# Kernel optimization log

Hardware: AMD Instinct MI355X
Metric: run time of the kernel (lower is better)

Reference implementation:

```python
import math
import jax, jax.numpy as jnp
import numpy as np

GRID_SIZE = 17
GRID_RANGE = 2.5
WIDTHS = [128, 256, 128]
LN_EPS = 1e-5

GRID = jnp.linspace(-GRID_RANGE, GRID_RANGE, GRID_SIZE, dtype=jnp.float32)
SPACING = jnp.float32(2.0 * GRID_RANGE / (GRID_SIZE - 1))


def _kan_layer(x, base_scale, spline_w, bias):
    # x: (B, I); base_scale: (I, O); spline_w: (I, O, G); bias: (O,)
    I = x.shape[-1]
    # degree-1 (hat) spline basis: (B, I, G)
    basis = jnp.clip(1.0 - jnp.abs(x[..., None] - GRID) / SPACING, 0.0, None)
    spline = jnp.einsum('big,iog->bio', basis, spline_w)          # (B, I, O)
    base = jax.nn.silu(x)[..., None] * base_scale[None]            # (B, I, O)
    edge = base + spline                                           # (B, I, O)
    out = edge.sum(axis=1) / math.sqrt(float(I)) + bias            # (B, O)
    return out, edge, basis


def _layer_norm(x, gamma, beta):
    mu = x.mean(axis=-1, keepdims=True)
    var = ((x - mu) ** 2).mean(axis=-1, keepdims=True)
    return (x - mu) * jax.lax.rsqrt(var + LN_EPS) * gamma + beta


def setup_inputs() -> dict:
    key = jax.random.key(0)
    ks = jax.random.split(key, 8)
    B = 4096
    I0, H, O = WIDTHS
    fan0 = 1.0 / math.sqrt(float(I0))
    fan1 = 1.0 / math.sqrt(float(H))
    return {
        'x': jax.random.normal(ks[0], (B, I0), dtype=jnp.float32),
        'base_scale0': fan0 * jax.random.normal(ks[1], (I0, H), dtype=jnp.float32),
        'spline_w0': 0.1 * fan0 * jax.random.normal(ks[2], (I0, H, GRID_SIZE), dtype=jnp.float32),
        'bias0': jnp.zeros((H,), dtype=jnp.float32),
        'base_scale1': fan1 * jax.random.normal(ks[3], (H, O), dtype=jnp.float32),
        'spline_w1': 0.1 * fan1 * jax.random.normal(ks[4], (H, O, GRID_SIZE), dtype=jnp.float32),
        'bias1': jnp.zeros((O,), dtype=jnp.float32),
        'ln_gamma': jnp.ones((H,), dtype=jnp.float32),
        'ln_beta': jnp.zeros((H,), dtype=jnp.float32),
    }


def reference(x, base_scale0, spline_w0, bias0, base_scale1, spline_w1, bias1, ln_gamma, ln_beta):
    h, _, _ = _kan_layer(x, base_scale0, spline_w0, bias0)
    h = _layer_norm(h, ln_gamma, ln_beta)
    out, edge1, basis1 = _kan_layer(h, base_scale1, spline_w1, bias1)
    # diagnostics on the last layer (mean/std, std unbiased=False)
    se_mean = edge1.mean()
    se_std = edge1.std()
    sb_mean = basis1.mean()
    sb_std = basis1.std()
    return out, edge1, basis1, se_mean, se_std, sb_mean, sb_std
```

## Files before the change

kernel.cpp:

```cpp
#include <hip/hip_runtime.h>

#define BATCH 4096
#define NI 128
#define NH 256
#define NO 128
#define NG 17

static constexpr size_t EDGE_OFF  = (size_t)BATCH * NO;
static constexpr size_t BASIS_OFF = EDGE_OFF + (size_t)BATCH * NH * NO;
static constexpr size_t SCAL_OFF  = BASIS_OFF + (size_t)BATCH * NH * NG;

typedef float  vf2 __attribute__((ext_vector_type(2)));
typedef float  vf4 __attribute__((ext_vector_type(4)));

__device__ __forceinline__ unsigned short f2bf(float v) {
    unsigned int b = __float_as_uint(v);
    b += 0x7FFFu + ((b >> 16) & 1u);
    return (unsigned short)(b >> 16);
}
__device__ __forceinline__ float bf2f(unsigned short u) {
    return __uint_as_float((unsigned int)u << 16);
}
__device__ __forceinline__ float2 bf2_to_f2(unsigned int v) {
    float2 r;
    r.x = __uint_as_float(v << 16);
    r.y = __uint_as_float(v & 0xFFFF0000u);
    return r;
}
__device__ __forceinline__ float4 bf4_to_f4(uint2 v) {
    float4 r;
    r.x = __uint_as_float(v.x << 16);
    r.y = __uint_as_float(v.x & 0xFFFF0000u);
    r.z = __uint_as_float(v.y << 16);
    r.w = __uint_as_float(v.y & 0xFFFF0000u);
    return r;
}

__device__ __forceinline__ void taps(float v, float& sil, float& wlo, float& whi,
                                     int& glo, int& ghi, float& u) {
    sil = v / (1.0f + __expf(-v));
    u   = (v + 2.5f) * 3.2f;
    float kf = floorf(u);
    int   k  = (int)kf;
    float f  = u - kf;
    wlo = 1.0f - f;  whi = f;
    glo = k;         ghi = k + 1;
    if (glo < 0 || glo > 16) { glo = 0; wlo = 0.0f; }
    if (ghi < 0 || ghi > 16) { ghi = 0; whi = 0.0f; }
}

__global__ __launch_bounds__(256) void transpose_convert(
    const float* __restrict__ w0, const float* __restrict__ w1,
    const float* __restrict__ bs1,
    unsigned short* __restrict__ w0t, unsigned short* __restrict__ w1t,
    unsigned short* __restrict__ bs1b) {
    int j = blockIdx.x * 256 + threadIdx.x;
    const int total0 = NI * NG * NH;
    const int total1 = NH * NG * NO;
    if (j < total0) {
        int i = j / (NG * NH);
        int r = j - i * (NG * NH);
        int g = r / NH;
        int o = r - g * NH;
        w0t[j] = f2bf(w0[((size_t)i * NH + o) * NG + g]);
    } else if (j < total0 + total1) {
        int jj = j - total0;
        int i = jj / (NG * NO);
        int r = jj - i * (NG * NO);
        int g = r / NO;
        int o = r - g * NO;
        w1t[jj] = f2bf(w1[((size_t)i * NO + o) * NG + g]);
    } else {
        int jj = j - total0 - total1;
        bs1b[jj] = f2bf(bs1[jj]);
    }
}

__global__ __launch_bounds__(128) void kan_fused(
    const float* __restrict__ x,
    const float* __restrict__ bs0,
    const float* __restrict__ bias0,
    const unsigned short* __restrict__ bs1,
    const float* __restrict__ bias1,
    const float* __restrict__ gamma,
    const float* __restrict__ beta,
    const unsigned short* __restrict__ w0t,
    const unsigned short* __restrict__ w1t,
    float* __restrict__ out,
    float4* __restrict__ partials)
{
    __shared__ float s_sil0[NI], s_wlo0[NI], s_whi0[NI];
    __shared__ int   s_gp0[NI];
    __shared__ float s_sil1[NH], s_wlo1[NH], s_whi1[NH], s_u1[NH];
    __shared__ int   s_glo1[NH], s_ghi1[NH];
    __shared__ float s_red[128];
    __shared__ float4 s_out4[128];
    __shared__ float4 s_red4[128];

    const int tid = threadIdx.x;
    const int b   = blockIdx.x;

    {
        float xv = x[(size_t)b * NI + tid];
        float sil, wlo, whi, u; int glo, ghi;
        taps(xv, sil, wlo, whi, glo, ghi, u);
        s_sil0[tid] = sil; s_wlo0[tid] = wlo; s_whi0[tid] = whi;
        s_gp0[tid] = glo | (ghi << 8);
    }
    __syncthreads();

    const int op = tid * 2;
    float h0 = 0.0f, h1 = 0.0f;
    for (int i = 0; i < NI; ++i) {
        const float sil = s_sil0[i], wlo = s_wlo0[i], whi = s_whi0[i];
        const unsigned int gp = (unsigned int)s_gp0[i];
        const float2 bsv = *reinterpret_cast<const float2*>(bs0 + (size_t)i * NH + op);
        const float2 wl  = bf2_to_f2(*reinterpret_cast<const unsigned int*>(w0t + ((size_t)i * NG + (gp & 0xffu)) * NH + op));
        const float2 wh  = bf2_to_f2(*reinterpret_cast<const unsigned int*>(w0t + ((size_t)i * NG + (gp >> 8)) * NH + op));
        h0 += sil * bsv.x + wlo * wl.x + whi * wh.x;
        h1 += sil * bsv.y + wlo * wl.y + whi * wh.y;
    }
    {
        const float2 b0 = *reinterpret_cast<const float2*>(bias0 + op);
        h0 = h0 * 0.08838834764831844f + b0.x;
        h1 = h1 * 0.08838834764831844f + b0.y;
    }

    s_red[tid] = h0 + h1;
    __syncthreads();
    for (int s = 64; s > 0; s >>= 1) {
        if (tid < s) s_red[tid] += s_red[tid + s];
        __syncthreads();
    }
    const float mu = s_red[0] * (1.0f / NH);
    __syncthreads();
    const float d0 = h0 - mu, d1 = h1 - mu;
    s_red[tid] = d0 * d0 + d1 * d1;
    __syncthreads();
    for (int s = 64; s > 0; s >>= 1) {
        if (tid < s) s_red[tid] += s_red[tid + s];
        __syncthreads();
    }
    const float rs = rsqrtf(s_red[0] * (1.0f / NH) + 1e-5f);
    __syncthreads();
    float hn0, hn1;
    {
        const float2 gm = *reinterpret_cast<const float2*>(gamma + op);
        const float2 bt = *reinterpret_cast<const float2*>(beta + op);
        hn0 = d0 * rs * gm.x + bt.x;
        hn1 = d1 * rs * gm.y + bt.y;
    }

    float bsum, bsq;
    {
        float sil, wlo, whi, u; int glo, ghi;
        taps(hn0, sil, wlo, whi, glo, ghi, u);
        s_sil1[op] = sil; s_wlo1[op] = wlo; s_whi1[op] = whi;
        s_glo1[op] = glo; s_ghi1[op] = ghi; s_u1[op] = u;
        bsum = wlo + whi;  bsq = wlo * wlo + whi * whi;
        taps(hn1, sil, wlo, whi, glo, ghi, u);
        s_sil1[op + 1] = sil; s_wlo1[op + 1] = wlo; s_whi1[op + 1] = whi;
        s_glo1[op + 1] = glo; s_ghi1[op + 1] = ghi; s_u1[op + 1] = u;
        bsum += wlo + whi; bsq += wlo * wlo + whi * whi;
    }
    __syncthreads();

    {
        float* bo = out + BASIS_OFF + (size_t)b * (NH * NG);
        #pragma unroll
        for (int it = 0; it < 17; ++it) {
            int f0 = (it * 128 + tid) * 2;
            int i0 = f0 / NG,       g0 = f0 - i0 * NG;
            int i1 = (f0 + 1) / NG, g1 = (f0 + 1) - i1 * NG;
            vf2 v;
            v.x = fmaxf(0.0f, 1.0f - fabsf(s_u1[i0] - (float)g0));
            v.y = fmaxf(0.0f, 1.0f - fabsf(s_u1[i1] - (float)g1));
            __builtin_nontemporal_store(v, reinterpret_cast<vf2*>(bo + f0));
        }
    }

    const int po = (tid & 31) * 4;
    const int q  = tid >> 5;
    float4 osum = make_float4(0.f, 0.f, 0.f, 0.f);
    float esq = 0.0f;
    float* eo = out + EDGE_OFF + (size_t)b * (NH * NO);
    #pragma unroll 2
    for (int it = 0; it < 64; ++it) {
        const int i = q * 64 + it;
        const float sil = s_sil1[i], wlo = s_wlo1[i], whi = s_whi1[i];
        const float4 bsv = bf4_to_f4(*reinterpret_cast<const uint2*>(bs1 + (size_t)i * NO + po));
        const float4 wl  = bf4_to_f4(*reinterpret_cast<const uint2*>(w1t + (size_t)(i * NG + s_glo1[i]) * NO + po));
        const float4 wh  = bf4_to_f4(*reinterpret_cast<const uint2*>(w1t + (size_t)(i * NG + s_ghi1[i]) * NO + po));
        vf4 e;
        e.x = sil * bsv.x + wlo * wl.x + whi * wh.x;
        e.y = sil * bsv.y + wlo * wl.y + whi * wh.y;
        e.z = sil * bsv.z + wlo * wl.z + whi * wh.z;
        e.w = sil * bsv.w + wlo * wl.w + whi * wh.w;
        __builtin_nontemporal_store(e, reinterpret_cast<vf4*>(eo + (size_t)i * NO + po));
        osum.x += e.x; osum.y += e.y; osum.z += e.z; osum.w += e.w;
        esq += e.x * e.x + e.y * e.y + e.z * e.z + e.w * e.w;
    }

    s_out4[tid] = osum;
    __syncthreads();
    if (tid < 32) {
        float4 a = s_out4[tid], b2 = s_out4[tid + 32], c = s_out4[tid + 64], d2 = s_out4[tid + 96];
        const float4 bi = *reinterpret_cast<const float4*>(bias1 + tid * 4);
        float4 o4;
        o4.x = (a.x + b2.x + c.x + d2.x) * 0.0625f + bi.x;
        o4.y = (a.y + b2.y + c.y + d2.y) * 0.0625f + bi.y;
        o4.z = (a.z + b2.z + c.z + d2.z) * 0.0625f + bi.z;
        o4.w = (a.w + b2.w + c.w + d2.w) * 0.0625f + bi.w;
        *reinterpret_cast<float4*>(out + (size_t)b * NO + tid * 4) = o4;
    }

    s_red4[tid] = make_float4(osum.x + osum.y + osum.z + osum.w, esq, bsum, bsq);
    __syncthreads();
    for (int s = 64; s > 0; s >>= 1) {
        if (tid < s) {
            float4 a = s_red4[tid], c = s_red4[tid + s];
            s_red4[tid] = make_float4(a.x + c.x, a.y + c.y, a.z + c.z, a.w + c.w);
        }
        __syncthreads();
    }
    if (tid == 0) partials[b] = s_red4[0];
}

__global__ __launch_bounds__(256) void finalize(const float4* __restrict__ partials,
                                                float* __restrict__ out) {
    __shared__ double red[256];
    const int tid = threadIdx.x;
    double a0 = 0, a1 = 0, a2 = 0, a3 = 0;
    for (int j = tid; j < BATCH; j += 256) {
        float4 p = partials[j];
        a0 += (double)p.x; a1 += (double)p.y; a2 += (double)p.z; a3 += (double)p.w;
    }
    double tot[4];
    double v[4] = {a0, a1, a2, a3};
    for (int c = 0; c < 4; ++c) {
        red[tid] = v[c];
        __syncthreads();
        for (int s = 128; s > 0; s >>= 1) {
            if (tid < s) red[tid] += red[tid + s];
            __syncthreads();
        }
        tot[c] = red[0];
        __syncthreads();
    }
    if (tid == 0) {
        const double Ne = (double)BATCH * NH * NO;
        const double Nb = (double)BATCH * NH * NG;
        double me = tot[0] / Ne;
        double ve = tot[1] / Ne - me * me;
        double mb = tot[2] / Nb;
        double vb = tot[3] / Nb - mb * mb;
        out[SCAL_OFF + 0] = (float)me;
        out[SCAL_OFF + 1] = (float)sqrt(ve > 0.0 ? ve : 0.0);
        out[SCAL_OFF + 2] = (float)mb;
        out[SCAL_OFF + 3] = (float)sqrt(vb > 0.0 ? vb : 0.0);
    }
}

extern "C" void kernel_launch(void* const* d_in, const int* in_sizes, int n_in,
                              void* d_out, int out_size, void* d_ws, size_t ws_size,
                              hipStream_t stream) {
    const float* x     = (const float*)d_in[0];
    const float* bs0   = (const float*)d_in[1];
    const float* w0    = (const float*)d_in[2];
    const float* bias0 = (const float*)d_in[3];
    const float* bs1   = (const float*)d_in[4];
    const float* w1    = (const float*)d_in[5];
    const float* bias1 = (const float*)d_in[6];
    const float* gamma = (const float*)d_in[7];
    const float* beta  = (const float*)d_in[8];
    float* out = (float*)d_out;

    unsigned short* w0t  = (unsigned short*)d_ws;
    unsigned short* w1t  = w0t + (size_t)NI * NG * NH;
    unsigned short* bs1b = w1t + (size_t)NH * NG * NO;
    size_t ofs = ((size_t)(NI * NG * NH) + (size_t)(NH * NG * NO) + NH * NO) * sizeof(unsigned short);
    ofs = (ofs + 15) & ~(size_t)15;
    float4* partials = (float4*)((char*)d_ws + ofs);

    hipLaunchKernelGGL(transpose_convert, dim3(4480), dim3(256), 0, stream,
                       w0, w1, bs1, w0t, w1t, bs1b);
    hipLaunchKernelGGL(kan_fused, dim3(BATCH), dim3(128), 0, stream,
                       x, bs0, bias0, bs1b, bias1, gamma, beta, w0t, w1t, out, partials);
    hipLaunchKernelGGL(finalize, dim3(1), dim3(256), 0, stream, partials, out);
}
```

Measured before the change: 166.0 us.

## Split fused KAN kernel into layer-0 and edge kernels via workspace buffer

Splits the single fused kernel into two launches. The first computes layer 0 plus LayerNorm and writes the normalized hidden vector to a workspace buffer. The second reads it back and computes the layer-1 edges, basis and partials. The aim is to lower per-kernel register and shared-memory pressure so each kernel can reach higher occupancy. The cost is an extra launch and a small global round trip for the hidden activations. The hidden-index mapping is also changed from interleaved pairs to tid and tid+128.

Result: slower. 173.7 us (+4.6%).

```diff
diff --git a/kernel.cpp b/kernel.cpp
--- a/kernel.cpp
+++ b/kernel.cpp
@@ -17,9 +17,6 @@
     unsigned int b = __float_as_uint(v);
     b += 0x7FFFu + ((b >> 16) & 1u);
     return (unsigned short)(b >> 16);
-}
-__device__ __forceinline__ float bf2f(unsigned short u) {
-    return __uint_as_float((unsigned int)u << 16);
 }
 __device__ __forceinline__ float2 bf2_to_f2(unsigned int v) {
     float2 r;
@@ -76,26 +73,18 @@
     }
 }
 
-__global__ __launch_bounds__(128) void kan_fused(
+__global__ __launch_bounds__(128) void kan_l0(
     const float* __restrict__ x,
     const float* __restrict__ bs0,
     const float* __restrict__ bias0,
-    const unsigned short* __restrict__ bs1,
-    const float* __restrict__ bias1,
     const float* __restrict__ gamma,
     const float* __restrict__ beta,
     const unsigned short* __restrict__ w0t,
-    const unsigned short* __restrict__ w1t,
-    float* __restrict__ out,
-    float4* __restrict__ partials)
+    float* __restrict__ hn)
 {
     __shared__ float s_sil0[NI], s_wlo0[NI], s_whi0[NI];
     __shared__ int   s_gp0[NI];
-    __shared__ float s_sil1[NH], s_wlo1[NH], s_whi1[NH], s_u1[NH];
-    __shared__ int   s_glo1[NH], s_ghi1[NH];
     __shared__ float s_red[128];
-    __shared__ float4 s_out4[128];
-    __shared__ float4 s_red4[128];
 
     const int tid = threadIdx.x;
     const int b   = blockIdx.x;
@@ -143,24 +132,44 @@
     }
     const float rs = rsqrtf(s_red[0] * (1.0f / NH) + 1e-5f);
     __syncthreads();
-    float hn0, hn1;
     {
         const float2 gm = *reinterpret_cast<const float2*>(gamma + op);
         const float2 bt = *reinterpret_cast<const float2*>(beta + op);
-        hn0 = d0 * rs * gm.x + bt.x;
-        hn1 = d1 * rs * gm.y + bt.y;
-    }
-
+        vf2 o;
+        o.x = d0 * rs * gm.x + bt.x;
+        o.y = d1 * rs * gm.y + bt.y;
+        *reinterpret_cast<vf2*>(hn + (size_t)b * NH + op) = o;
+    }
+}
+
+__global__ __launch_bounds__(128) void kan_edge(
+    const float* __restrict__ hn,
+    const unsigned short* __restrict__ bs1,
+    const float* __restrict__ bias1,
+    const unsigned short* __restrict__ w1t,
+    float* __restrict__ out,
+    float4* __restrict__ partials)
+{
+    __shared__ float s_sil1[NH], s_wlo1[NH], s_whi1[NH], s_u1[NH];
+    __shared__ int   s_glo1[NH], s_ghi1[NH];
+    __shared__ float4 s_out4[128];
+    __shared__ float4 s_red4[128];
+
+    const int tid = threadIdx.x;
+    const int b   = blockIdx.x;
+
+    const float hn0 = hn[(size_t)b * NH + tid];
+    const float hn1 = hn[(size_t)b * NH + tid + 128];
     float bsum, bsq;
     {
         float sil, wlo, whi, u; int glo, ghi;
         taps(hn0, sil, wlo, whi, glo, ghi, u);
-        s_sil1[op] = sil; s_wlo1[op] = wlo; s_whi1[op] = whi;
-        s_glo1[op] = glo; s_ghi1[op] = ghi; s_u1[op] = u;
+        s_sil1[tid] = sil; s_wlo1[tid] = wlo; s_whi1[tid] = whi;
+        s_glo1[tid] = glo; s_ghi1[tid] = ghi; s_u1[tid] = u;
         bsum = wlo + whi;  bsq = wlo * wlo + whi * whi;
         taps(hn1, sil, wlo, whi, glo, ghi, u);
-        s_sil1[op + 1] = sil; s_wlo1[op + 1] = wlo; s_whi1[op + 1] = whi;
-        s_glo1[op + 1] = glo; s_ghi1[op + 1] = ghi; s_u1[op + 1] = u;
+        s_sil1[tid + 128] = sil; s_wlo1[tid + 128] = wlo; s_whi1[tid + 128] = whi;
+        s_glo1[tid + 128] = glo; s_ghi1[tid + 128] = ghi; s_u1[tid + 128] = u;
         bsum += wlo + whi; bsq += wlo * wlo + whi * whi;
     }
     __syncthreads();
@@ -281,10 +290,13 @@
     size_t ofs = ((size_t)(NI * NG * NH) + (size_t)(NH * NG * NO) + NH * NO) * sizeof(unsigned short);
     ofs = (ofs + 15) & ~(size_t)15;
     float4* partials = (float4*)((char*)d_ws + ofs);
+    float*  hnbuf    = (float*)((char*)d_ws + ofs + BATCH * sizeof(float4));
 
     hipLaunchKernelGGL(transpose_convert, dim3(4480), dim3(256), 0, stream,
                        w0, w1, bs1, w0t, w1t, bs1b);
-    hipLaunchKernelGGL(kan_fused, dim3(BATCH), dim3(128), 0, stream,
-                       x, bs0, bias0, bs1b, bias1, gamma, beta, w0t, w1t, out, partials);
+    hipLaunchKernelGGL(kan_l0, dim3(BATCH), dim3(128), 0, stream,
+                       x, bs0, bias0, gamma, beta, w0t, hnbuf);
+    hipLaunchKernelGGL(kan_edge, dim3(BATCH), dim3(128), 0, stream,
+                       hnbuf, bs1b, bias1, w1t, out, partials);
     hipLaunchKernelGGL(finalize, dim3(1), dim3(256), 0, stream, partials, out);
 }
```

## Split layer 0 into a dense MFMA GEMM over the full hat-basis expansion

Applied to the files above, without the earlier changes.

Layer 0 is moved out of the per-row fused kernel into a new kernel. It handles 16 batch rows per block, builds the dense 128x17 hat-basis matrix on the fly in bf16 and multiplies it against pre-tiled bf16 spline weights using MFMA 16x16x32 instructions. The SiLU base term is computed with fp32 FMAs, and the result is written to a workspace buffer that the fused kernel reads back. This swaps sparse two-tap gathers, which reload the weights for every row, for dense matrix-core work with reuse across 16 rows. The cost is one extra launch, a global round trip for the hidden activations, bf16 rounding of the basis values, and many MFMAs on zero basis entries.

After: 179.7 us. 1.08x slower.

```diff
diff --git a/kernel.cpp b/kernel.cpp
--- a/kernel.cpp
+++ b/kernel.cpp
@@ -5,6 +5,7 @@
 #define NH 256
 #define NO 128
 #define NG 17
+#define K0 2176
 
 static constexpr size_t EDGE_OFF  = (size_t)BATCH * NO;
 static constexpr size_t BASIS_OFF = EDGE_OFF + (size_t)BATCH * NH * NO;
@@ -12,20 +13,13 @@
 
 typedef float  vf2 __attribute__((ext_vector_type(2)));
 typedef float  vf4 __attribute__((ext_vector_type(4)));
+typedef short  bf16x8 __attribute__((ext_vector_type(8)));
+typedef float  f32x4 __attribute__((ext_vector_type(4)));
 
 __device__ __forceinline__ unsigned short f2bf(float v) {
     unsigned int b = __float_as_uint(v);
     b += 0x7FFFu + ((b >> 16) & 1u);
     return (unsigned short)(b >> 16);
-}
-__device__ __forceinline__ float bf2f(unsigned short u) {
-    return __uint_as_float((unsigned int)u << 16);
-}
-__device__ __forceinline__ float2 bf2_to_f2(unsigned int v) {
-    float2 r;
-    r.x = __uint_as_float(v << 16);
-    r.y = __uint_as_float(v & 0xFFFF0000u);
-    return r;
 }
 __device__ __forceinline__ float4 bf4_to_f4(uint2 v) {
     float4 r;
@@ -52,45 +46,112 @@
 __global__ __launch_bounds__(256) void transpose_convert(
     const float* __restrict__ w0, const float* __restrict__ w1,
     const float* __restrict__ bs1,
-    unsigned short* __restrict__ w0t, unsigned short* __restrict__ w1t,
+    unsigned short* __restrict__ w0B, unsigned short* __restrict__ w1t,
     unsigned short* __restrict__ bs1b) {
     int j = blockIdx.x * 256 + threadIdx.x;
-    const int total0 = NI * NG * NH;
+    const int n0 = K0 / 32 * NH;
     const int total1 = NH * NG * NO;
-    if (j < total0) {
-        int i = j / (NG * NH);
-        int r = j - i * (NG * NH);
-        int g = r / NH;
-        int o = r - g * NH;
-        w0t[j] = f2bf(w0[((size_t)i * NH + o) * NG + g]);
-    } else if (j < total0 + total1) {
-        int jj = j - total0;
+    if (j < n0) {
+        const int kt = j >> 8;
+        const int o  = j & 255;
+        unsigned short* dst = w0B + (size_t)kt * 8192 + o * 32;
+        #pragma unroll
+        for (int kl = 0; kl < 32; ++kl) {
+            unsigned int k = kt * 32 + kl;
+            unsigned int i = (k * 3856u) >> 16;
+            unsigned int g = k - 17u * i;
+            dst[kl] = f2bf(w0[((size_t)i * NH + o) * NG + g]);
+        }
+    } else if (j < n0 + total1) {
+        int jj = j - n0;
         int i = jj / (NG * NO);
         int r = jj - i * (NG * NO);
         int g = r / NO;
         int o = r - g * NO;
         w1t[jj] = f2bf(w1[((size_t)i * NO + o) * NG + g]);
-    } else {
-        int jj = j - total0 - total1;
+    } else if (j < n0 + total1 + NH * NO) {
+        int jj = j - n0 - total1;
         bs1b[jj] = f2bf(bs1[jj]);
     }
 }
 
-__global__ __launch_bounds__(128) void kan_fused(
+__global__ __launch_bounds__(512) void layer0_gemm(
     const float* __restrict__ x,
     const float* __restrict__ bs0,
+    const unsigned short* __restrict__ w0B,
+    float* __restrict__ hsum)
+{
+    __shared__ float s_u[16 * 129];
+    __shared__ float s_sil[16 * NI];
+    __shared__ float s_hb[16 * NH];
+    const int tid = threadIdx.x;
+    const int rb  = blockIdx.x * 16;
+
+    for (int j = tid; j < 16 * NI; j += 512) {
+        const int r = j >> 7, c = j & 127;
+        float xv = x[(size_t)rb * NI + j];
+        s_sil[j] = xv / (1.0f + __expf(-xv));
+        s_u[r * 129 + c] = (xv + 2.5f) * 3.2f;
+    }
+    __syncthreads();
+
+    {
+        const int o  = tid & 255;
+        const int r0 = (tid >> 8) * 8;
+        float acc[8] = {};
+        #pragma unroll 4
+        for (int k = 0; k < NI; ++k) {
+            float bv = bs0[(size_t)k * NH + o];
+            #pragma unroll
+            for (int r = 0; r < 8; ++r) acc[r] += s_sil[(r0 + r) * NI + k] * bv;
+        }
+        #pragma unroll
+        for (int r = 0; r < 8; ++r) s_hb[(r0 + r) * NH + o] = acc[r];
+    }
+    __syncthreads();
+
+    const int lane = tid & 63;
+    const int wave = tid >> 6;
+    const int r    = lane & 15;
+    const int kg   = lane >> 4;
+    const int o0   = (wave * 2 + 0) * 16 + (lane & 15);
+    const int o1   = (wave * 2 + 1) * 16 + (lane & 15);
+    f32x4 acc0 = {0.f, 0.f, 0.f, 0.f}, acc1 = {0.f, 0.f, 0.f, 0.f};
+    for (int kt = 0; kt < K0 / 32; ++kt) {
+        const int k0 = kt * 32 + kg * 8;
+        bf16x8 av;
+        #pragma unroll
+        for (int j = 0; j < 8; ++j) {
+            unsigned int k = k0 + j;
+            unsigned int i = (k * 3856u) >> 16;
+            float g = (float)(k - 17u * i);
+            float v = fmaxf(0.0f, 1.0f - fabsf(s_u[r * 129 + i] - g));
+            av[j] = (short)f2bf(v);
+        }
+        const bf16x8 bv0 = *reinterpret_cast<const bf16x8*>(w0B + (size_t)kt * 8192 + o0 * 32 + kg * 8);
+        const bf16x8 bv1 = *reinterpret_cast<const bf16x8*>(w0B + (size_t)kt * 8192 + o1 * 32 + kg * 8);
+        acc0 = __builtin_amdgcn_mfma_f32_16x16x32_bf16(av, bv0, acc0, 0, 0, 0);
+        acc1 = __builtin_amdgcn_mfma_f32_16x16x32_bf16(av, bv1, acc1, 0, 0, 0);
+    }
+    #pragma unroll
+    for (int reg = 0; reg < 4; ++reg) {
+        const int row = kg * 4 + reg;
+        hsum[(size_t)(rb + row) * NH + o0] = acc0[reg] + s_hb[row * NH + o0];
+        hsum[(size_t)(rb + row) * NH + o1] = acc1[reg] + s_hb[row * NH + o1];
+    }
+}
+
+__global__ __launch_bounds__(128) void kan_fused(
+    const float* __restrict__ hsum,
     const float* __restrict__ bias0,
     const unsigned short* __restrict__ bs1,
     const float* __restrict__ bias1,
     const float* __restrict__ gamma,
     const float* __restrict__ beta,
-    const unsigned short* __restrict__ w0t,
     const unsigned short* __restrict__ w1t,
     float* __restrict__ out,
     float4* __restrict__ partials)
 {
-    __shared__ float s_sil0[NI], s_wlo0[NI], s_whi0[NI];
-    __shared__ int   s_gp0[NI];
     __shared__ float s_sil1[NH], s_wlo1[NH], s_whi1[NH], s_u1[NH];
     __shared__ int   s_glo1[NH], s_ghi1[NH];
     __shared__ float s_red[128];
@@ -100,30 +161,13 @@
     const int tid = threadIdx.x;
     const int b   = blockIdx.x;
 
-    {
-        float xv = x[(size_t)b * NI + tid];
-        float sil, wlo, whi, u; int glo, ghi;
-        taps(xv, sil, wlo, whi, glo, ghi, u);
-        s_sil0[tid] = sil; s_wlo0[tid] = wlo; s_whi0[tid] = whi;
-        s_gp0[tid] = glo | (ghi << 8);
-    }
-    __syncthreads();
-
     const int op = tid * 2;
-    float h0 = 0.0f, h1 = 0.0f;
-    for (int i = 0; i < NI; ++i) {
-        const float sil = s_sil0[i], wlo = s_wlo0[i], whi = s_whi0[i];
-        const unsigned int gp = (unsigned int)s_gp0[i];
-        const float2 bsv = *reinterpret_cast<const float2*>(bs0 + (size_t)i * NH + op);
-        const float2 wl  = bf2_to_f2(*reinterpret_cast<const unsigned int*>(w0t + ((size_t)i * NG + (gp & 0xffu)) * NH + op));
-        const float2 wh  = bf2_to_f2(*reinterpret_cast<const unsigned int*>(w0t + ((size_t)i * NG + (gp >> 8)) * NH + op));
-        h0 += sil * bsv.x + wlo * wl.x + whi * wh.x;
-        h1 += sil * bsv.y + wlo * wl.y + whi * wh.y;
-    }
-    {
+    float h0, h1;
+    {
+        const float2 hs = *reinterpret_cast<const float2*>(hsum + (size_t)b * NH + op);
         const float2 b0 = *reinterpret_cast<const float2*>(bias0 + op);
-        h0 = h0 * 0.08838834764831844f + b0.x;
-        h1 = h1 * 0.08838834764831844f + b0.y;
+        h0 = hs.x * 0.08838834764831844f + b0.x;
+        h1 = hs.y * 0.08838834764831844f + b0.y;
     }
 
     s_red[tid] = h0 + h1;
@@ -275,16 +319,19 @@
     const float* beta  = (const float*)d_in[8];
     float* out = (float*)d_out;
 
-    unsigned short* w0t  = (unsigned short*)d_ws;
-    unsigned short* w1t  = w0t + (size_t)NI * NG * NH;
+    unsigned short* w0B  = (unsigned short*)d_ws;
+    unsigned short* w1t  = w0B + (size_t)K0 * NH;
     unsigned short* bs1b = w1t + (size_t)NH * NG * NO;
-    size_t ofs = ((size_t)(NI * NG * NH) + (size_t)(NH * NG * NO) + NH * NO) * sizeof(unsigned short);
+    size_t ofs = ((size_t)(K0 * NH) + (size_t)(NH * NG * NO) + NH * NO) * sizeof(unsigned short);
     ofs = (ofs + 15) & ~(size_t)15;
     float4* partials = (float4*)((char*)d_ws + ofs);
-
-    hipLaunchKernelGGL(transpose_convert, dim3(4480), dim3(256), 0, stream,
-                       w0, w1, bs1, w0t, w1t, bs1b);
+    float*  hsum     = (float*)((char*)d_ws + ofs + BATCH * sizeof(float4));
+
+    hipLaunchKernelGGL(transpose_convert, dim3(2372), dim3(256), 0, stream,
+                       w0, w1, bs1, w0B, w1t, bs1b);
+    hipLaunchKernelGGL(layer0_gemm, dim3(BATCH / 16), dim3(512), 0, stream,
+                       x, bs0, w0B, hsum);
     hipLaunchKernelGGL(kan_fused, dim3(BATCH), dim3(128), 0, stream,
-                       x, bs0, bias0, bs1b, bias1, gamma, beta, w0t, w1t, out, partials);
+                       hsum, bias0, bs1b, bias1, gamma, beta, w1t, out, partials);
     hipLaunchKernelGGL(finalize, dim3(1), dim3(256), 0, stream, partials, out);
 }
```
